# Optimization experiments

Hardware: AMD Instinct MI355X
Metric: run time of the kernel (lower is better)

Reference implementation:

```python
import jax, jax.numpy as jnp
import numpy as np

D_MODEL = 768
NUM_HEADS = 12
D_K = D_MODEL // NUM_HEADS


def setup_inputs() -> dict:
    key = jax.random.key(0)
    ks = jax.random.split(key, 7)
    B, S = 4, 2048
    query = jax.random.normal(ks[0], (B, S, D_MODEL), dtype=jnp.float32)
    key_t = jax.random.normal(ks[1], (B, S, D_MODEL), dtype=jnp.float32)
    value = jax.random.normal(ks[2], (B, S, D_MODEL), dtype=jnp.float32)
    lim = 1.0 / np.sqrt(D_MODEL)
    Wq = jax.random.uniform(ks[3], (D_MODEL, D_MODEL), jnp.float32, -lim, lim)  # torch Linear weight [out,in]
    bq = jax.random.uniform(ks[4], (D_MODEL,), jnp.float32, -lim, lim)
    Wo = jax.random.uniform(ks[5], (D_MODEL, D_MODEL), jnp.float32, -lim, lim)
    bo = jax.random.uniform(ks[6], (D_MODEL,), jnp.float32, -lim, lim)
    return {"query": query, "key": key_t, "value": value,
            "Wq": Wq, "bq": bq, "Wo": Wo, "bo": bo}


def _proj_heads(x, W, b):
    # x: [B,S,D] -> [B,H,S,d_k]; torch Linear: x @ W.T + b
    B, S, _ = x.shape
    y = x @ W.T + b
    return y.reshape(B, S, NUM_HEADS, D_K).transpose(0, 2, 1, 3)


def reference(query, key, value, Wq, bq, Wo, bo):
    # Faithful to source: linear_q is used for q, k AND v (source bug).
    q = _proj_heads(query, Wq, bq)
    k = _proj_heads(key, Wq, bq)
    v = _proj_heads(value, Wq, bq)
    scale = 1.0 / jnp.sqrt(jnp.asarray(D_K, q.dtype))
    scores = jnp.einsum('bhqd,bhkd->bhqk', q, k) * scale  # [B,H,S,S]
    attn = jax.nn.softmax(scores, axis=-1)
    out = jnp.einsum('bhqk,bhkd->bhqd', attn, v)  # [B,H,S,d_k]
    B, H, S, dk = out.shape
    out = out.transpose(0, 2, 1, 3).reshape(B, S, H * dk)
    return out @ Wo.T + bo
```

## Files before the change

kernel.cpp:

```cpp
#include <hip/hip_runtime.h>
#include <math.h>

typedef _Float16 f16x8 __attribute__((ext_vector_type(8)));
typedef _Float16 f16x4 __attribute__((ext_vector_type(4)));
typedef float    f32x4 __attribute__((ext_vector_type(4)));
typedef unsigned short us4 __attribute__((ext_vector_type(4)));

constexpr int DM = 768, NH = 12, DK = 64, SEQ = 2048, BB = 4;
constexpr int MROWS = BB * SEQ;
constexpr size_t XELE = (size_t)MROWS * DM;
constexpr size_t WELE = (size_t)DM * DM;

constexpr size_t OFF_X16  = 0;
constexpr size_t OFF_W16  = 3 * XELE;
constexpr size_t OFF_WO16 = OFF_W16 + WELE;
constexpr size_t OFF_QKV  = OFF_WO16 + WELE;
constexpr size_t OFF_ATT  = OFF_QKV + 3 * XELE;
constexpr size_t TOT_CVT  = OFF_QKV;


constexpr float QSCALE = 0.125f * 1.44269504f;

__device__ __forceinline__ void gload16(const _Float16* g, _Float16* l) {
    __builtin_amdgcn_global_load_lds(
        (const __attribute__((address_space(1))) unsigned int*)g,
        (__attribute__((address_space(3))) unsigned int*)l, 16, 0, 0);
}

__global__ __launch_bounds__(256) void cvt_kernel(
    const float* __restrict__ q, const float* __restrict__ k,
    const float* __restrict__ v, const float* __restrict__ wq,
    const float* __restrict__ wo, _Float16* __restrict__ dst)
{
    const size_t i = ((size_t)blockIdx.x * 256 + threadIdx.x) * 4;
    if (i >= TOT_CVT) return;
    const float* src; size_t base;
    if      (i < XELE)            { src = q;  base = 0; }
    else if (i < 2 * XELE)        { src = k;  base = XELE; }
    else if (i < 3 * XELE)        { src = v;  base = 2 * XELE; }
    else if (i < OFF_WO16)        { src = wq; base = OFF_W16; }
    else                          { src = wo; base = OFF_WO16; }
    const float4 f = *(const float4*)(src + (i - base));
    _Float16 h4[4] = {(_Float16)f.x, (_Float16)f.y, (_Float16)f.z, (_Float16)f.w};
    *(us4*)(dst + i) = *(us4*)h4;
}

template <int MODE>
__global__ __launch_bounds__(256) void mfma_gemm(
    const _Float16* __restrict__ Xbase, const _Float16* __restrict__ Wmat,
    const float* __restrict__ bias, void* __restrict__ Yout)
{
    __shared__ _Float16 smem[(MODE == 0) ? 128 * 136 : 16384];

    const int tid  = threadIdx.x;
    const int w    = tid >> 6, lane = tid & 63;
    const int cl   = lane & 15;
    const int g    = lane >> 4;
    const int m0   = blockIdx.y * 128, n0 = blockIdx.x * 128;
    const int z    = blockIdx.z;
    const _Float16* X = Xbase + (size_t)z * XELE;

    const int wr = w >> 1, wc = w & 1;
    const int lrow = lane >> 2;
    const int lcol = (lane & 3) * 8;

    f32x4 acc[4][4] = {};

    constexpr int NK = DM / 32;
#pragma unroll
    for (int t = 0; t < 2; ++t) {
        const int c = w + t * 4;
        gload16(X    + (size_t)(m0 + c * 16 + lrow) * DM + lcol, &smem[c * 512]);
        gload16(Wmat + (size_t)(n0 + c * 16 + lrow) * DM + lcol, &smem[4096 + c * 512]);
    }

    int cur = 0;
    for (int ki = 0; ki < NK; ++ki) {
        __syncthreads();
        if (ki + 1 < NK) {
            const int kn = (ki + 1) * 32;
            _Float16* dst = &smem[(cur ^ 1) * 8192];
#pragma unroll
            for (int t = 0; t < 2; ++t) {
                const int c = w + t * 4;
                gload16(X    + (size_t)(m0 + c * 16 + lrow) * DM + kn + lcol, &dst[c * 512]);
                gload16(Wmat + (size_t)(n0 + c * 16 + lrow) * DM + kn + lcol, &dst[4096 + c * 512]);
            }
        }
        const _Float16* As = &smem[cur * 8192];
        const _Float16* Bs = As + 4096;

        f16x8 a[4], bfr[4];
#pragma unroll
        for (int mt = 0; mt < 4; ++mt)
            a[mt] = *(const f16x8*)&As[(wr * 64 + mt * 16 + cl) * 32 + g * 8];
#pragma unroll
        for (int nt = 0; nt < 4; ++nt)
            bfr[nt] = *(const f16x8*)&Bs[(wc * 64 + nt * 16 + cl) * 32 + g * 8];
#pragma unroll
        for (int mt = 0; mt < 4; ++mt)
#pragma unroll
            for (int nt = 0; nt < 4; ++nt)
                acc[mt][nt] = __builtin_amdgcn_mfma_f32_16x16x32_f16(
                    a[mt], bfr[nt], acc[mt][nt], 0, 0, 0);
        cur ^= 1;
    }

    if (MODE == 1) {
#pragma unroll
        for (int nt = 0; nt < 4; ++nt) {
            const int col = n0 + wc * 64 + nt * 16 + cl;
            const float bv = bias[col];
#pragma unroll
            for (int mt = 0; mt < 4; ++mt)
#pragma unroll
                for (int r = 0; r < 4; ++r) {
                    const int row = m0 + wr * 64 + mt * 16 + g * 4 + r;
                    ((float*)Yout)[(size_t)row * DM + col] = acc[mt][nt][r] + bv;
                }
        }
        return;
    }

    __syncthreads();
    const float sc = (z == 0) ? QSCALE : 1.0f;
#pragma unroll
    for (int nt = 0; nt < 4; ++nt) {
        const int col = wc * 64 + nt * 16 + cl;
        const float bv = bias[n0 + col];
#pragma unroll
        for (int mt = 0; mt < 4; ++mt)
#pragma unroll
            for (int r = 0; r < 4; ++r) {
                const int row = wr * 64 + mt * 16 + g * 4 + r;
                const _Float16 hv = (_Float16)((acc[mt][nt][r] + bv) * sc);
                if (z == 2) smem[col * 136 + row] = hv;
                else        smem[row * 136 + col] = hv;
            }
    }
    __syncthreads();

    _Float16* Yz = (_Float16*)Yout + (size_t)z * XELE;
#pragma unroll
    for (int it = 0; it < 8; ++it) {
        const int idx = tid + it * 256;
        const int row = idx >> 4;
        const int grp = idx & 15;
        const f16x8 vv = *(const f16x8*)&smem[row * 136 + grp * 8];
        if (z == 2) {
            const int f  = n0 + row, hh = f >> 6, d = f & 63;
            const int gm = m0 + grp * 8;
            const int bb = gm >> 11, s = gm & (SEQ - 1);
            const int ssw = (s & ~63) | ((((s >> 3) & 7) ^ (d & 7)) << 3);
            *(f16x8*)&Yz[(((size_t)bb * NH + hh) * DK + d) * SEQ + ssw] = vv;
        } else {
            const int gm = m0 + row;
            const int bb = gm >> 11, s = gm & (SEQ - 1);
            const int n  = n0 + grp * 8, hh = n >> 6, d0 = n & 63;
            const int dsw = ((((d0 >> 3) ^ (s & 7)) & 7) << 3);
            *(f16x8*)&Yz[(((size_t)bb * NH + hh) * SEQ + s) * DK + dsw] = vv;
        }
    }
}

__global__ __launch_bounds__(256) void flash3(
    const _Float16* __restrict__ qkv, _Float16* __restrict__ attno)
{
    __shared__ _Float16 KsB[2 * 64 * 64];
    __shared__ _Float16 VtB[2 * 64 * 64];
    __shared__ _Float16 Ps[128 * 72];

    const int tid = threadIdx.x;
    const int w = tid >> 6, lane = tid & 63;
    const int cl = lane & 15, g = lane >> 4;
    const int swz = cl & 7;
    const int q0 = blockIdx.x * 128;
    const int h  = blockIdx.y, b = blockIdx.z;

    const size_t headoff = ((size_t)b * NH + h) * SEQ * DK;
    const _Float16* Qg = qkv + headoff;
    const _Float16* Kg = qkv + XELE + headoff;
    const _Float16* Vg = qkv + 2 * XELE + headoff;

    const int ldr = lane >> 3, ldc = (lane & 7) * 8;

#pragma unroll
    for (int t = 0; t < 2; ++t) {
        const int c = w * 2 + t;
        gload16(Kg + (size_t)(c * 8 + ldr) * DK + ldc, &KsB[c * 512]);
        gload16(Vg + (size_t)(c * 8 + ldr) * SEQ + ldc, &VtB[c * 512]);
    }

    f16x8 qf[2][2];
#pragma unroll
    for (int qt = 0; qt < 2; ++qt)
#pragma unroll
        for (int ks = 0; ks < 2; ++ks)
            qf[qt][ks] = *(const f16x8*)(
                Qg + (size_t)(q0 + w * 32 + qt * 16 + cl) * DK
                   + (((ks * 4 + g) ^ swz) << 3));

    float m_run[2] = {-1e30f, -1e30f};
    float l_run[2] = {0.f, 0.f};
    f32x4 acc[2][4] = {};

    int cur = 0;
    for (int j0 = 0; j0 < SEQ; j0 += 64) {
        __syncthreads();
        if (j0 + 64 < SEQ) {
            const int jn = j0 + 64;
            _Float16* Kd = &KsB[(cur ^ 1) * 4096];
            _Float16* Vd = &VtB[(cur ^ 1) * 4096];
#pragma unroll
            for (int t = 0; t < 2; ++t) {
                const int c = w * 2 + t;
                gload16(Kg + (size_t)(jn + c * 8 + ldr) * DK + ldc, &Kd[c * 512]);
                gload16(Vg + (size_t)(c * 8 + ldr) * SEQ + jn + ldc, &Vd[c * 512]);
            }
        }
        const _Float16* Ks = &KsB[cur * 4096];
        const _Float16* Vt = &VtB[cur * 4096];

        f16x8 kf[4][2];
#pragma unroll
        for (int kt = 0; kt < 4; ++kt)
#pragma unroll
            for (int ks = 0; ks < 2; ++ks)
                kf[kt][ks] = *(const f16x8*)&Ks[(kt * 16 + cl) * 64
                                                + (((ks * 4 + g) ^ swz) << 3)];

        f32x4 st[2][4];
#pragma unroll
        for (int qt = 0; qt < 2; ++qt)
#pragma unroll
            for (int kt = 0; kt < 4; ++kt) {
                f32x4 s = {};
#pragma unroll
                for (int ks = 0; ks < 2; ++ks)
                    s = __builtin_amdgcn_mfma_f32_16x16x32_f16(
                        kf[kt][ks], qf[qt][ks], s, 0, 0, 0);
                st[qt][kt] = s;
            }

#pragma unroll
        for (int qt = 0; qt < 2; ++qt) {
            float mx = st[qt][0][0];
#pragma unroll
            for (int kt = 0; kt < 4; ++kt)
#pragma unroll
                for (int r = 0; r < 4; ++r) mx = fmaxf(mx, st[qt][kt][r]);
            mx = fmaxf(mx, __shfl_xor(mx, 16));
            mx = fmaxf(mx, __shfl_xor(mx, 32));
            const float mo = m_run[qt];
            const float mn = fmaxf(mo, mx);
            const float al = __builtin_amdgcn_exp2f(mo - mn);
            m_run[qt] = mn;

            float ps = 0.f;
            const int prow = w * 32 + qt * 16 + cl;
#pragma unroll
            for (int kt = 0; kt < 4; ++kt) {
                float p0 = __builtin_amdgcn_exp2f(st[qt][kt][0] - mn);
                float p1 = __builtin_amdgcn_exp2f(st[qt][kt][1] - mn);
                float p2 = __builtin_amdgcn_exp2f(st[qt][kt][2] - mn);
                float p3 = __builtin_amdgcn_exp2f(st[qt][kt][3] - mn);
                ps += (p0 + p1) + (p2 + p3);
                f16x4 pk = {(_Float16)p0, (_Float16)p1, (_Float16)p2, (_Float16)p3};
                *(f16x4*)&Ps[(size_t)prow * 72 + kt * 16 + g * 4] = pk;
            }
            ps += __shfl_xor(ps, 16);
            ps += __shfl_xor(ps, 32);
            l_run[qt] = l_run[qt] * al + ps;
#pragma unroll
            for (int dt = 0; dt < 4; ++dt)
#pragma unroll
                for (int r = 0; r < 4; ++r) acc[qt][dt][r] *= al;
        }

        f16x8 vf[4][2], pf[2][2];
#pragma unroll
        for (int dt = 0; dt < 4; ++dt)
#pragma unroll
            for (int ks = 0; ks < 2; ++ks)
                vf[dt][ks] = *(const f16x8*)&Vt[(dt * 16 + cl) * 64
                                                + (((ks * 4 + g) ^ swz) << 3)];
#pragma unroll
        for (int qt = 0; qt < 2; ++qt)
#pragma unroll
            for (int ks = 0; ks < 2; ++ks)
                pf[qt][ks] = *(const f16x8*)&Ps[(size_t)(w * 32 + qt * 16 + cl) * 72
                                                + ks * 32 + g * 8];
#pragma unroll
        for (int qt = 0; qt < 2; ++qt)
#pragma unroll
            for (int ks = 0; ks < 2; ++ks)
#pragma unroll
                for (int dt = 0; dt < 4; ++dt)
                    acc[qt][dt] = __builtin_amdgcn_mfma_f32_16x16x32_f16(
                        vf[dt][ks], pf[qt][ks], acc[qt][dt], 0, 0, 0);
        cur ^= 1;
    }

#pragma unroll
    for (int qt = 0; qt < 2; ++qt) {
        const float inv = 1.0f / l_run[qt];
        const int q = q0 + w * 32 + qt * 16 + cl;
#pragma unroll
        for (int dt = 0; dt < 4; ++dt) {
            f16x4 pk = {(_Float16)(acc[qt][dt][0] * inv),
                        (_Float16)(acc[qt][dt][1] * inv),
                        (_Float16)(acc[qt][dt][2] * inv),
                        (_Float16)(acc[qt][dt][3] * inv)};
            *(f16x4*)&attno[((size_t)b * SEQ + q) * DM + h * DK + dt * 16 + g * 4] = pk;
        }
    }
}

extern "C" void kernel_launch(void* const* d_in, const int* in_sizes, int n_in,
                              void* d_out, int out_size, void* d_ws, size_t ws_size,
                              hipStream_t stream) {
    const float* q  = (const float*)d_in[0];
    const float* k  = (const float*)d_in[1];
    const float* v  = (const float*)d_in[2];
    const float* Wq = (const float*)d_in[3];
    const float* bq = (const float*)d_in[4];
    const float* Wo = (const float*)d_in[5];
    const float* bo = (const float*)d_in[6];

    _Float16* ws16  = (_Float16*)d_ws;
    _Float16* x16   = ws16 + OFF_X16;
    _Float16* w16   = ws16 + OFF_W16;
    _Float16* wo16  = ws16 + OFF_WO16;
    _Float16* qkv16 = ws16 + OFF_QKV;
    _Float16* att16 = ws16 + OFF_ATT;

    cvt_kernel<<<(int)(TOT_CVT / 1024), 256, 0, stream>>>(q, k, v, Wq, Wo, ws16);

    mfma_gemm<0><<<dim3(DM / 128, MROWS / 128, 3), 256, 0, stream>>>(
        x16, w16, bq, qkv16);

    flash3<<<dim3(SEQ / 128, NH, BB), 256, 0, stream>>>(qkv16, att16);

    mfma_gemm<1><<<dim3(DM / 128, MROWS / 128, 1), 256, 0, stream>>>(
        att16, wo16, bo, (float*)d_out);
}
```

Measured before the change: 298.6 us.

## Remap block indices for XCD-aware L2 locality and pack fp16 conversions

Replaces 3D grids with 1D grids whose block IDs are decoded so that consecutive blocks (round-robined across the 8 XCDs) share weight tiles or head K/V data in each XCD's L2. The GEMMs group 8 M-blocks per XCD slot and flash groups heads/batches so each XCD repeatedly streams the same K/V. It also switches fp32→fp16 packing to cvt_pkrtz, which uses round-toward-zero instead of round-to-nearest, and hoists the LDS row offsets for P. The rounding change slightly alters numerics.

```diff
diff --git a/kernel.cpp b/kernel.cpp
--- a/kernel.cpp
+++ b/kernel.cpp
@@ -3,8 +3,10 @@
 
 typedef _Float16 f16x8 __attribute__((ext_vector_type(8)));
 typedef _Float16 f16x4 __attribute__((ext_vector_type(4)));
+typedef __fp16   hf2   __attribute__((ext_vector_type(2)));
 typedef float    f32x4 __attribute__((ext_vector_type(4)));
 typedef unsigned short us4 __attribute__((ext_vector_type(4)));
+typedef unsigned int u32;
 
 constexpr int DM = 768, NH = 12, DK = 64, SEQ = 2048, BB = 4;
 constexpr int MROWS = BB * SEQ;
@@ -25,6 +27,13 @@
     __builtin_amdgcn_global_load_lds(
         (const __attribute__((address_space(1))) unsigned int*)g,
         (__attribute__((address_space(3))) unsigned int*)l, 16, 0, 0);
+}
+
+__device__ __forceinline__ uint2 pack4(float a, float b, float c, float d) {
+    uint2 r;
+    r.x = __builtin_bit_cast(u32, __builtin_amdgcn_cvt_pkrtz(a, b));
+    r.y = __builtin_bit_cast(u32, __builtin_amdgcn_cvt_pkrtz(c, d));
+    return r;
 }
 
 __global__ __launch_bounds__(256) void cvt_kernel(
@@ -52,12 +61,19 @@
 {
     __shared__ _Float16 smem[(MODE == 0) ? 128 * 136 : 16384];
 
+    const int bid = blockIdx.x;
+    const int xs  = bid & 7;
+    const int rr  = bid >> 3;
+    const int m_blk = ((rr & 7) << 3) | xs;
+    const int tt  = rr >> 3;
+    const int n_blk = (MODE == 0) ? (tt % 6) : tt;
+    const int z     = (MODE == 0) ? (tt / 6) : 0;
+
     const int tid  = threadIdx.x;
     const int w    = tid >> 6, lane = tid & 63;
     const int cl   = lane & 15;
     const int g    = lane >> 4;
-    const int m0   = blockIdx.y * 128, n0 = blockIdx.x * 128;
-    const int z    = blockIdx.z;
+    const int m0   = m_blk * 128, n0 = n_blk * 128;
     const _Float16* X = Xbase + (size_t)z * XELE;
 
     const int wr = w >> 1, wc = w & 1;
@@ -170,12 +186,18 @@
     __shared__ _Float16 VtB[2 * 64 * 64];
     __shared__ _Float16 Ps[128 * 72];
 
+    const int bid = blockIdx.x;
+    const int xs  = bid & 7;
+    const int rr  = bid >> 3;
+    const int p   = (rr % 6) * 8 + xs;
+    const int qtb = rr / 6;
+    const int h   = p % NH, b = p / NH;
+    const int q0  = qtb * 128;
+
     const int tid = threadIdx.x;
     const int w = tid >> 6, lane = tid & 63;
     const int cl = lane & 15, g = lane >> 4;
     const int swz = cl & 7;
-    const int q0 = blockIdx.x * 128;
-    const int h  = blockIdx.y, b = blockIdx.z;
 
     const size_t headoff = ((size_t)b * NH + h) * SEQ * DK;
     const _Float16* Qg = qkv + headoff;
@@ -203,6 +225,11 @@
     float m_run[2] = {-1e30f, -1e30f};
     float l_run[2] = {0.f, 0.f};
     f32x4 acc[2][4] = {};
+
+    int psbase[2];
+#pragma unroll
+    for (int qt = 0; qt < 2; ++qt)
+        psbase[qt] = (w * 32 + qt * 16 + cl) * 72;
 
     int cur = 0;
     for (int j0 = 0; j0 < SEQ; j0 += 64) {
@@ -257,7 +284,6 @@
             m_run[qt] = mn;
 
             float ps = 0.f;
-            const int prow = w * 32 + qt * 16 + cl;
 #pragma unroll
             for (int kt = 0; kt < 4; ++kt) {
                 float p0 = __builtin_amdgcn_exp2f(st[qt][kt][0] - mn);
@@ -265,8 +291,7 @@
                 float p2 = __builtin_amdgcn_exp2f(st[qt][kt][2] - mn);
                 float p3 = __builtin_amdgcn_exp2f(st[qt][kt][3] - mn);
                 ps += (p0 + p1) + (p2 + p3);
-                f16x4 pk = {(_Float16)p0, (_Float16)p1, (_Float16)p2, (_Float16)p3};
-                *(f16x4*)&Ps[(size_t)prow * 72 + kt * 16 + g * 4] = pk;
+                *(uint2*)&Ps[psbase[qt] + kt * 16 + g * 4] = pack4(p0, p1, p2, p3);
             }
             ps += __shfl_xor(ps, 16);
             ps += __shfl_xor(ps, 32);
@@ -288,8 +313,7 @@
         for (int qt = 0; qt < 2; ++qt)
 #pragma unroll
             for (int ks = 0; ks < 2; ++ks)
-                pf[qt][ks] = *(const f16x8*)&Ps[(size_t)(w * 32 + qt * 16 + cl) * 72
-                                                + ks * 32 + g * 8];
+                pf[qt][ks] = *(const f16x8*)&Ps[psbase[qt] + ks * 32 + g * 8];
 #pragma unroll
         for (int qt = 0; qt < 2; ++qt)
 #pragma unroll
@@ -307,11 +331,9 @@
         const int q = q0 + w * 32 + qt * 16 + cl;
 #pragma unroll
         for (int dt = 0; dt < 4; ++dt) {
-            f16x4 pk = {(_Float16)(acc[qt][dt][0] * inv),
-                        (_Float16)(acc[qt][dt][1] * inv),
-                        (_Float16)(acc[qt][dt][2] * inv),
-                        (_Float16)(acc[qt][dt][3] * inv)};
-            *(f16x4*)&attno[((size_t)b * SEQ + q) * DM + h * DK + dt * 16 + g * 4] = pk;
+            uint2 pk = pack4(acc[qt][dt][0] * inv, acc[qt][dt][1] * inv,
+                             acc[qt][dt][2] * inv, acc[qt][dt][3] * inv);
+            *(uint2*)&attno[((size_t)b * SEQ + q) * DM + h * DK + dt * 16 + g * 4] = pk;
         }
     }
 }
@@ -336,11 +358,9 @@
 
     cvt_kernel<<<(int)(TOT_CVT / 1024), 256, 0, stream>>>(q, k, v, Wq, Wo, ws16);
 
-    mfma_gemm<0><<<dim3(DM / 128, MROWS / 128, 3), 256, 0, stream>>>(
-        x16, w16, bq, qkv16);
-
-    flash3<<<dim3(SEQ / 128, NH, BB), 256, 0, stream>>>(qkv16, att16);
-
-    mfma_gemm<1><<<dim3(DM / 128, MROWS / 128, 1), 256, 0, stream>>>(
-        att16, wo16, bo, (float*)d_out);
-}
+    mfma_gemm<0><<<1152, 256, 0, stream>>>(x16, w16, bq, qkv16);
+
+    flash3<<<768, 256, 0, stream>>>(qkv16, att16);
+
+    mfma_gemm<1><<<384, 256, 0, stream>>>(att16, wo16, bo, (float*)d_out);
+}
```

After: 271.1 us. 9.2% less time.
